# Performance work log

Measured on AMD Instinct MI355X. Metric: run time of the kernel, lower is better.

Reference implementation:

```python
import jax, jax.numpy as jnp
import numpy as np

E = 16
TOP_K = 2


def setup_inputs() -> dict:
    key = jax.random.key(0)
    k1, k2, k3, k4, k5 = jax.random.split(key, 5)
    H, I = 2048, 1408
    scale = 0.02  # typical init scale, keeps activations numerically tame
    return {
        "hidden_states": jax.random.normal(k1, (4, 2048, H), dtype=jnp.float32),
        "gate_w": jax.random.normal(k2, (H, E), dtype=jnp.float32) * scale,
        "w1": jax.random.normal(k3, (E, H, I), dtype=jnp.float32) * scale,
        "w3": jax.random.normal(k4, (E, H, I), dtype=jnp.float32) * scale,
        "w2": jax.random.normal(k5, (E, I, H), dtype=jnp.float32) * scale,
    }


def reference(hidden_states, gate_w, w1, w3, w2):
    orig_shape = hidden_states.shape
    H = orig_shape[-1]
    x = hidden_states.reshape(-1, H)          # [T, H]
    T = x.shape[0]

    # Router: gate linear -> softmax -> top-k -> renormalize (norm_expert_weight=True)
    router_logits = x @ gate_w                # [T, E]
    probs = jax.nn.softmax(router_logits, axis=-1)
    topk_w, topk_i = jax.lax.top_k(probs, TOP_K)          # [T, K]
    topk_w = topk_w / jnp.sum(topk_w, axis=-1, keepdims=True)

    # Dense combine weights [T, E] (zero for non-selected experts)
    combine = jnp.zeros((T, E), dtype=x.dtype)
    combine = combine.at[jnp.arange(T)[:, None], topk_i].add(topk_w)

    # Grouped SwiGLU experts: out = sum_e combine[:, e] * ((silu(x@w1_e) * (x@w3_e)) @ w2_e)
    out = jnp.zeros_like(x)
    for e in range(E):  # fixed small expert count
        gate_act = jax.nn.silu(x @ w1[e])     # [T, I]
        up = x @ w3[e]                        # [T, I]
        y = (gate_act * up) @ w2[e]           # [T, H]
        out = out + combine[:, e:e + 1] * y

    return out.reshape(orig_shape)
```

## Files before the change

### kernel.cpp

```cpp
#include <hip/hip_runtime.h>
#include <hip/hip_bf16.h>

#define E_ 16
#define H_ 2048
#define I_ 1408
#define BM 128
#define BN 128
#define BK 32
#define SB 48

typedef __attribute__((ext_vector_type(8))) short bf16x8;
typedef __attribute__((ext_vector_type(4))) float f32x4;

__device__ __forceinline__ int swz(int row, int e) {
  return row * SB + ((((e >> 3) + (row >> 2)) & 3) << 3) + (e & 7);
}

__device__ __forceinline__ unsigned int pk2(float a, float b) {
  __hip_bfloat162 h = __float22bfloat162_rn(make_float2(a, b));
  unsigned int u;
  __builtin_memcpy(&u, &h, 4);
  return u;
}

__device__ __forceinline__ unsigned short bf16b(float a) {
  unsigned int u = __builtin_bit_cast(unsigned int, a);
  u = (u + 0x7fffu + ((u >> 16) & 1u)) >> 16;
  return (unsigned short)u;
}

__global__ __launch_bounds__(64) void moe_router(
    const float* __restrict__ x, const float* __restrict__ gw,
    int* __restrict__ counts, int* __restrict__ list2s,
    float* __restrict__ listw, int T)
{
  const int lane = threadIdx.x;
  const int t0 = blockIdx.x * 4;
  double acc[4][16];
#pragma unroll
  for (int i = 0; i < 4; ++i)
#pragma unroll
    for (int j = 0; j < 16; ++j) acc[i][j] = 0.0;

  const float4* gw4 = (const float4*)gw;
  for (int it = 0; it < H_ / 64; ++it) {
    const int h = it * 64 + lane;
    float gv[16];
    *(float4*)&gv[0]  = gw4[h * 4 + 0];
    *(float4*)&gv[4]  = gw4[h * 4 + 1];
    *(float4*)&gv[8]  = gw4[h * 4 + 2];
    *(float4*)&gv[12] = gw4[h * 4 + 3];
    float xr[4];
#pragma unroll
    for (int i = 0; i < 4; ++i) xr[i] = x[(size_t)(t0 + i) * H_ + h];
#pragma unroll
    for (int i = 0; i < 4; ++i) {
      const double xv = (double)xr[i];
#pragma unroll
      for (int j = 0; j < 16; ++j) acc[i][j] += xv * (double)gv[j];
    }
  }
#pragma unroll
  for (int i = 0; i < 4; ++i)
#pragma unroll
    for (int j = 0; j < 16; ++j) {
      double v = acc[i][j];
#pragma unroll
      for (int m = 32; m > 0; m >>= 1) v += __shfl_xor(v, m, 64);
      acc[i][j] = v;
    }
  if (lane == 0) {
#pragma unroll
    for (int i = 0; i < 4; ++i) {
      const int t = t0 + i;
      double b1 = -1e300, b2 = -1e300;
      int i1 = 0, i2 = 0;
#pragma unroll
      for (int j = 0; j < 16; ++j) {
        const double l = acc[i][j];
        if (l > b1) { b2 = b1; i2 = i1; b1 = l; i1 = j; }
        else if (l > b2) { b2 = l; i2 = j; }
      }
      const float ex = expf((float)(b2 - b1));
      const float wa = 1.f / (1.f + ex);
      const float wb = ex / (1.f + ex);
      int p = atomicAdd(&counts[i1], 1);
      list2s[i1 * T + p] = t * 2;
      listw[i1 * T + p] = wa;
      p = atomicAdd(&counts[i2], 1);
      list2s[i2 * T + p] = t * 2 + 1;
      listw[i2 * T + p] = wb;
    }
  }
}

__global__ __launch_bounds__(256) void convert_x(
    const float* __restrict__ x, unsigned short* __restrict__ xb)
{
  const size_t idx = ((size_t)blockIdx.x * 256 + threadIdx.x) * 8;
  const float4 f0 = *(const float4*)(x + idx);
  const float4 f1 = *(const float4*)(x + idx + 4);
  uint4 o;
  o.x = pk2(f0.x, f0.y); o.y = pk2(f0.z, f0.w);
  o.z = pk2(f1.x, f1.y); o.w = pk2(f1.z, f1.w);
  *(uint4*)(xb + idx) = o;
}

__global__ __launch_bounds__(256) void convert_wT(
    const float* __restrict__ src, unsigned short* __restrict__ dst,
    int R, int C)
{
  const int e = blockIdx.z;
  src += (size_t)e * R * C;
  dst += (size_t)e * C * R;
  const int r0 = blockIdx.y * 128 + (threadIdx.x >> 4) * 8;
  const int c0 = blockIdx.x * 128 + (threadIdx.x & 15) * 8;
  float av[8][8];
#pragma unroll
  for (int j = 0; j < 8; ++j) {
    const float4 t0 = *(const float4*)(src + (size_t)(r0 + j) * C + c0);
    const float4 t1 = *(const float4*)(src + (size_t)(r0 + j) * C + c0 + 4);
    av[j][0] = t0.x; av[j][1] = t0.y; av[j][2] = t0.z; av[j][3] = t0.w;
    av[j][4] = t1.x; av[j][5] = t1.y; av[j][6] = t1.z; av[j][7] = t1.w;
  }
#pragma unroll
  for (int n = 0; n < 8; ++n) {
    uint4 o;
    o.x = pk2(av[0][n], av[1][n]);
    o.y = pk2(av[2][n], av[3][n]);
    o.z = pk2(av[4][n], av[5][n]);
    o.w = pk2(av[6][n], av[7][n]);
    *(uint4*)(dst + (size_t)(c0 + n) * R + r0) = o;
  }
}

__global__ __launch_bounds__(256) void moe_gemm1_b16(
    const unsigned short* __restrict__ xb, const unsigned short* __restrict__ w1b,
    const unsigned short* __restrict__ w3b, const int* __restrict__ counts,
    const int* __restrict__ list2s, unsigned short* __restrict__ act, int T)
{
  const int e = blockIdx.z;
  const int cnt = counts[e];
  const int m0 = blockIdx.y * BM;
  if (m0 >= cnt) return;
  const int n0 = blockIdx.x * BN;
  const unsigned short* w1e = w1b + (size_t)e * H_ * I_;
  const unsigned short* w3e = w3b + (size_t)e * H_ * I_;
  const int* lst = list2s + (size_t)e * T;

  __shared__ unsigned short As[BM * SB], B1s[BN * SB], B3s[BN * SB];

  const int tid = threadIdx.x;
  const int lane = tid & 63, wave = tid >> 6;
  const int wr = (wave >> 1) * 64, wc = (wave & 1) * 64;
  const int l16 = lane & 15, quad = lane >> 4;

  const int ar = tid >> 1, ahalf = tid & 1;
  const int apos = m0 + ar;
  const int a_t2s = lst[apos < cnt ? apos : cnt - 1];
  const unsigned short* aptr = xb + (size_t)(a_t2s >> 1) * H_ + ahalf * 16;
  const unsigned short* b1p = w1e + (size_t)(n0 + ar) * H_ + ahalf * 16;
  const unsigned short* b3p = w3e + (size_t)(n0 + ar) * H_ + ahalf * 16;

  f32x4 acc1[4][4], acc3[4][4];
  const f32x4 fz = {0.f, 0.f, 0.f, 0.f};
#pragma unroll
  for (int mi = 0; mi < 4; ++mi)
#pragma unroll
    for (int ni = 0; ni < 4; ++ni) { acc1[mi][ni] = fz; acc3[mi][ni] = fz; }

  uint4 pA0, pA1, pB10, pB11, pB30, pB31;
  pA0  = *(const uint4*)(aptr);     pA1  = *(const uint4*)(aptr + 8);
  pB10 = *(const uint4*)(b1p);      pB11 = *(const uint4*)(b1p + 8);
  pB30 = *(const uint4*)(b3p);      pB31 = *(const uint4*)(b3p + 8);

  for (int k0 = 0; k0 < H_; k0 += BK) {
    __syncthreads();
    *(uint4*)&As[swz(ar, ahalf * 16)]      = pA0;
    *(uint4*)&As[swz(ar, ahalf * 16 + 8)]  = pA1;
    *(uint4*)&B1s[swz(ar, ahalf * 16)]     = pB10;
    *(uint4*)&B1s[swz(ar, ahalf * 16 + 8)] = pB11;
    *(uint4*)&B3s[swz(ar, ahalf * 16)]     = pB30;
    *(uint4*)&B3s[swz(ar, ahalf * 16 + 8)] = pB31;
    const int kn = (k0 + BK < H_) ? k0 + BK : 0;
    pA0  = *(const uint4*)(aptr + kn);     pA1  = *(const uint4*)(aptr + kn + 8);
    pB10 = *(const uint4*)(b1p + kn);      pB11 = *(const uint4*)(b1p + kn + 8);
    pB30 = *(const uint4*)(b3p + kn);      pB31 = *(const uint4*)(b3p + kn + 8);
    __syncthreads();

    bf16x8 af[4], b1f[4], b3f[4];
#pragma unroll
    for (int mi = 0; mi < 4; ++mi)
      af[mi] = *(const bf16x8*)&As[swz(wr + mi * 16 + l16, quad * 8)];
#pragma unroll
    for (int ni = 0; ni < 4; ++ni) {
      b1f[ni] = *(const bf16x8*)&B1s[swz(wc + ni * 16 + l16, quad * 8)];
      b3f[ni] = *(const bf16x8*)&B3s[swz(wc + ni * 16 + l16, quad * 8)];
    }
#pragma unroll
    for (int mi = 0; mi < 4; ++mi)
#pragma unroll
      for (int ni = 0; ni < 4; ++ni) {
        acc1[mi][ni] = __builtin_amdgcn_mfma_f32_16x16x32_bf16(af[mi], b1f[ni], acc1[mi][ni], 0, 0, 0);
        acc3[mi][ni] = __builtin_amdgcn_mfma_f32_16x16x32_bf16(af[mi], b3f[ni], acc3[mi][ni], 0, 0, 0);
      }
  }

#pragma unroll
  for (int mi = 0; mi < 4; ++mi) {
    const int rbase = m0 + wr + mi * 16 + quad * 4;
#pragma unroll
    for (int r = 0; r < 4; ++r) {
      const int pos = rbase + r;
      if (pos < cnt) {
        const int t2s = lst[pos];
        unsigned short* op = act + (size_t)t2s * I_ + n0 + wc + l16;
#pragma unroll
        for (int ni = 0; ni < 4; ++ni) {
          const float g = acc1[mi][ni][r];
          const float u = acc3[mi][ni][r];
          const float s = g / (1.f + __expf(-g));
          op[ni * 16] = bf16b(s * u);
        }
      }
    }
  }
}

__global__ __launch_bounds__(256) void moe_gemm2_b16(
    const unsigned short* __restrict__ act, const unsigned short* __restrict__ w2b,
    const int* __restrict__ counts, const int* __restrict__ list2s,
    const float* __restrict__ listw, float* __restrict__ out, int T)
{
  const int e = blockIdx.z;
  const int cnt = counts[e];
  const int m0 = blockIdx.y * BM;
  if (m0 >= cnt) return;
  const int n0 = blockIdx.x * BN;
  const unsigned short* w2e = w2b + (size_t)e * I_ * H_;
  const int* lst = list2s + (size_t)e * T;
  const float* lw = listw + (size_t)e * T;

  __shared__ unsigned short As[BM * SB], Bs[BN * SB];

  const int tid = threadIdx.x;
  const int lane = tid & 63, wave = tid >> 6;
  const int wr = (wave >> 1) * 64, wc = (wave & 1) * 64;
  const int l16 = lane & 15, quad = lane >> 4;

  const int ar = tid >> 1, ahalf = tid & 1;
  const int apos = m0 + ar;
  const int a_t2s = lst[apos < cnt ? apos : cnt - 1];
  const unsigned short* aptr = act + (size_t)a_t2s * I_ + ahalf * 16;
  const unsigned short* bp = w2e + (size_t)(n0 + ar) * I_ + ahalf * 16;

  f32x4 acc[4][4];
  const f32x4 fz = {0.f, 0.f, 0.f, 0.f};
#pragma unroll
  for (int mi = 0; mi < 4; ++mi)
#pragma unroll
    for (int ni = 0; ni < 4; ++ni) acc[mi][ni] = fz;

  uint4 pA0, pA1, pB0, pB1;
  pA0 = *(const uint4*)(aptr);  pA1 = *(const uint4*)(aptr + 8);
  pB0 = *(const uint4*)(bp);    pB1 = *(const uint4*)(bp + 8);

  for (int k0 = 0; k0 < I_; k0 += BK) {
    __syncthreads();
    *(uint4*)&As[swz(ar, ahalf * 16)]     = pA0;
    *(uint4*)&As[swz(ar, ahalf * 16 + 8)] = pA1;
    *(uint4*)&Bs[swz(ar, ahalf * 16)]     = pB0;
    *(uint4*)&Bs[swz(ar, ahalf * 16 + 8)] = pB1;
    const int kn = (k0 + BK < I_) ? k0 + BK : 0;
    pA0 = *(const uint4*)(aptr + kn);  pA1 = *(const uint4*)(aptr + kn + 8);
    pB0 = *(const uint4*)(bp + kn);    pB1 = *(const uint4*)(bp + kn + 8);
    __syncthreads();

    bf16x8 af[4], bf[4];
#pragma unroll
    for (int mi = 0; mi < 4; ++mi)
      af[mi] = *(const bf16x8*)&As[swz(wr + mi * 16 + l16, quad * 8)];
#pragma unroll
    for (int ni = 0; ni < 4; ++ni)
      bf[ni] = *(const bf16x8*)&Bs[swz(wc + ni * 16 + l16, quad * 8)];
#pragma unroll
    for (int mi = 0; mi < 4; ++mi)
#pragma unroll
      for (int ni = 0; ni < 4; ++ni)
        acc[mi][ni] = __builtin_amdgcn_mfma_f32_16x16x32_bf16(af[mi], bf[ni], acc[mi][ni], 0, 0, 0);
  }

#pragma unroll
  for (int mi = 0; mi < 4; ++mi) {
    const int rbase = m0 + wr + mi * 16 + quad * 4;
#pragma unroll
    for (int r = 0; r < 4; ++r) {
      const int pos = rbase + r;
      if (pos < cnt) {
        const int t2s = lst[pos];
        const float wt = lw[pos];
        float* op = out + (size_t)(t2s >> 1) * H_ + n0 + wc + l16;
#pragma unroll
        for (int ni = 0; ni < 4; ++ni)
          atomicAdd(op + ni * 16, wt * acc[mi][ni][r]);
      }
    }
  }
}

__device__ __forceinline__ void stage_b(const float* __restrict__ bp,
                                        unsigned short* Bs, int bn, int bk, int ldb) {
  const float4 r0 = *(const float4*)(bp);
  const float4 r1 = *(const float4*)(bp + ldb);
  const float4 r2 = *(const float4*)(bp + 2 * ldb);
  const float4 r3 = *(const float4*)(bp + 3 * ldb);
  uint2 c;
  c.x = pk2(r0.x, r1.x); c.y = pk2(r2.x, r3.x);
  *(uint2*)&Bs[swz(bn + 0, bk)] = c;
  c.x = pk2(r0.y, r1.y); c.y = pk2(r2.y, r3.y);
  *(uint2*)&Bs[swz(bn + 1, bk)] = c;
  c.x = pk2(r0.z, r1.z); c.y = pk2(r2.z, r3.z);
  *(uint2*)&Bs[swz(bn + 2, bk)] = c;
  c.x = pk2(r0.w, r1.w); c.y = pk2(r2.w, r3.w);
  *(uint2*)&Bs[swz(bn + 3, bk)] = c;
}

__global__ __launch_bounds__(256) void moe_gemm1_f32(
    const float* __restrict__ x, const float* __restrict__ w1,
    const float* __restrict__ w3, const int* __restrict__ counts,
    const int* __restrict__ list2s, unsigned short* __restrict__ act, int T)
{
  const int e = blockIdx.z;
  const int cnt = counts[e];
  const int m0 = blockIdx.y * BM;
  if (m0 >= cnt) return;
  const int n0 = blockIdx.x * BN;
  const float* w1e = w1 + (size_t)e * H_ * I_;
  const float* w3e = w3 + (size_t)e * H_ * I_;
  const int* lst = list2s + (size_t)e * T;

  __shared__ unsigned short As[BM * SB], B1s[BN * SB], B3s[BN * SB];

  const int tid = threadIdx.x;
  const int lane = tid & 63, wave = tid >> 6;
  const int wr = (wave >> 1) * 64, wc = (wave & 1) * 64;
  const int l16 = lane & 15, quad = lane >> 4;

  const int ar = tid >> 1, ahalf = tid & 1;
  const int apos = m0 + ar;
  const int a_t2s = lst[apos < cnt ? apos : cnt - 1];
  const float* aptr = x + (size_t)(a_t2s >> 1) * H_ + ahalf * 16;

  const int nq = tid & 31, kb = tid >> 5;
  const int bn = nq * 4, bk = kb * 4;

  f32x4 acc1[4][4], acc3[4][4];
  const f32x4 fz = {0.f, 0.f, 0.f, 0.f};
#pragma unroll
  for (int mi = 0; mi < 4; ++mi)
#pragma unroll
    for (int ni = 0; ni < 4; ++ni) { acc1[mi][ni] = fz; acc3[mi][ni] = fz; }

  for (int k0 = 0; k0 < H_; k0 += BK) {
    __syncthreads();
    {
      const float4 a0 = *(const float4*)(aptr + k0);
      const float4 a1 = *(const float4*)(aptr + k0 + 4);
      const float4 a2 = *(const float4*)(aptr + k0 + 8);
      const float4 a3 = *(const float4*)(aptr + k0 + 12);
      uint4 A0, A1;
      A0.x = pk2(a0.x, a0.y); A0.y = pk2(a0.z, a0.w);
      A0.z = pk2(a1.x, a1.y); A0.w = pk2(a1.z, a1.w);
      A1.x = pk2(a2.x, a2.y); A1.y = pk2(a2.z, a2.w);
      A1.z = pk2(a3.x, a3.y); A1.w = pk2(a3.z, a3.w);
      *(uint4*)&As[swz(ar, ahalf * 16)] = A0;
      *(uint4*)&As[swz(ar, ahalf * 16 + 8)] = A1;
    }
    stage_b(w1e + (size_t)(k0 + bk) * I_ + n0 + bn, B1s, bn, bk, I_);
    stage_b(w3e + (size_t)(k0 + bk) * I_ + n0 + bn, B3s, bn, bk, I_);
    __syncthreads();

    bf16x8 af[4], b1f[4], b3f[4];
#pragma unroll
    for (int mi = 0; mi < 4; ++mi)
      af[mi] = *(const bf16x8*)&As[swz(wr + mi * 16 + l16, quad * 8)];
#pragma unroll
    for (int ni = 0; ni < 4; ++ni) {
      b1f[ni] = *(const bf16x8*)&B1s[swz(wc + ni * 16 + l16, quad * 8)];
      b3f[ni] = *(const bf16x8*)&B3s[swz(wc + ni * 16 + l16, quad * 8)];
    }
#pragma unroll
    for (int mi = 0; mi < 4; ++mi)
#pragma unroll
      for (int ni = 0; ni < 4; ++ni) {
        acc1[mi][ni] = __builtin_amdgcn_mfma_f32_16x16x32_bf16(af[mi], b1f[ni], acc1[mi][ni], 0, 0, 0);
        acc3[mi][ni] = __builtin_amdgcn_mfma_f32_16x16x32_bf16(af[mi], b3f[ni], acc3[mi][ni], 0, 0, 0);
      }
  }

#pragma unroll
  for (int mi = 0; mi < 4; ++mi) {
    const int rbase = m0 + wr + mi * 16 + quad * 4;
#pragma unroll
    for (int r = 0; r < 4; ++r) {
      const int pos = rbase + r;
      if (pos < cnt) {
        const int t2s = lst[pos];
        unsigned short* op = act + (size_t)t2s * I_ + n0 + wc + l16;
#pragma unroll
        for (int ni = 0; ni < 4; ++ni) {
          const float g = acc1[mi][ni][r];
          const float u = acc3[mi][ni][r];
          const float s = g / (1.f + __expf(-g));
          op[ni * 16] = bf16b(s * u);
        }
      }
    }
  }
}

__global__ __launch_bounds__(256) void moe_gemm2_f32(
    const unsigned short* __restrict__ act, const float* __restrict__ w2,
    const int* __restrict__ counts, const int* __restrict__ list2s,
    const float* __restrict__ listw, float* __restrict__ out, int T)
{
  const int e = blockIdx.z;
  const int cnt = counts[e];
  const int m0 = blockIdx.y * BM;
  if (m0 >= cnt) return;
  const int n0 = blockIdx.x * BN;
  const float* w2e = w2 + (size_t)e * I_ * H_;
  const int* lst = list2s + (size_t)e * T;
  const float* lw = listw + (size_t)e * T;

  __shared__ unsigned short As[BM * SB], Bs[BN * SB];

  const int tid = threadIdx.x;
  const int lane = tid & 63, wave = tid >> 6;
  const int wr = (wave >> 1) * 64, wc = (wave & 1) * 64;
  const int l16 = lane & 15, quad = lane >> 4;

  const int ar = tid >> 1, ahalf = tid & 1;
  const int apos = m0 + ar;
  const int a_t2s = lst[apos < cnt ? apos : cnt - 1];
  const unsigned short* aptr = act + (size_t)a_t2s * I_ + ahalf * 16;

  const int nq = tid & 31, kb = tid >> 5;
  const int bn = nq * 4, bk = kb * 4;

  f32x4 acc[4][4];
  const f32x4 fz = {0.f, 0.f, 0.f, 0.f};
#pragma unroll
  for (int mi = 0; mi < 4; ++mi)
#pragma unroll
    for (int ni = 0; ni < 4; ++ni) acc[mi][ni] = fz;

  for (int k0 = 0; k0 < I_; k0 += BK) {
    __syncthreads();
    {
      const uint4 A0 = *(const uint4*)(aptr + k0);
      const uint4 A1 = *(const uint4*)(aptr + k0 + 8);
      *(uint4*)&As[swz(ar, ahalf * 16)] = A0;
      *(uint4*)&As[swz(ar, ahalf * 16 + 8)] = A1;
    }
    stage_b(w2e + (size_t)(k0 + bk) * H_ + n0 + bn, Bs, bn, bk, H_);
    __syncthreads();

    bf16x8 af[4], bf[4];
#pragma unroll
    for (int mi = 0; mi < 4; ++mi)
      af[mi] = *(const bf16x8*)&As[swz(wr + mi * 16 + l16, quad * 8)];
#pragma unroll
    for (int ni = 0; ni < 4; ++ni)
      bf[ni] = *(const bf16x8*)&Bs[swz(wc + ni * 16 + l16, quad * 8)];
#pragma unroll
    for (int mi = 0; mi < 4; ++mi)
#pragma unroll
      for (int ni = 0; ni < 4; ++ni)
        acc[mi][ni] = __builtin_amdgcn_mfma_f32_16x16x32_bf16(af[mi], bf[ni], acc[mi][ni], 0, 0, 0);
  }

#pragma unroll
  for (int mi = 0; mi < 4; ++mi) {
    const int rbase = m0 + wr + mi * 16 + quad * 4;
#pragma unroll
    for (int r = 0; r < 4; ++r) {
      const int pos = rbase + r;
      if (pos < cnt) {
        const int t2s = lst[pos];
        const float wt = lw[pos];
        float* op = out + (size_t)(t2s >> 1) * H_ + n0 + wc + l16;
#pragma unroll
        for (int ni = 0; ni < 4; ++ni)
          atomicAdd(op + ni * 16, wt * acc[mi][ni][r]);
      }
    }
  }
}

extern "C" void kernel_launch(void* const* d_in, const int* in_sizes, int n_in,
                              void* d_out, int out_size, void* d_ws, size_t ws_size,
                              hipStream_t stream) {
  const float* x  = (const float*)d_in[0];
  const float* gw = (const float*)d_in[1];
  const float* w1 = (const float*)d_in[2];
  const float* w3 = (const float*)d_in[3];
  const float* w2 = (const float*)d_in[4];
  float* out = (float*)d_out;
  const int T = in_sizes[0] / H_;

  char* ws = (char*)d_ws;
  int* counts = (int*)ws;
  int* list2s = (int*)(ws + 256);
  float* listw = (float*)(ws + 256 + (size_t)E_ * T * 4);
  const size_t o_act = 256 + 2 * (size_t)E_ * T * 4;
  unsigned short* act = (unsigned short*)(ws + o_act);
  const size_t o_xb  = o_act + 2 * (size_t)T * I_ * 2;
  const size_t whi   = (size_t)E_ * H_ * I_ * 2;
  const size_t o_w1b = o_xb + (size_t)T * H_ * 2;
  const size_t o_w3b = o_w1b + whi;
  const size_t o_w2b = o_w3b + whi;
  const size_t need  = o_w2b + whi;

  hipMemsetAsync(counts, 0, 256, stream);
  hipMemsetAsync(out, 0, (size_t)out_size * sizeof(float), stream);
  moe_router<<<T / 4, 64, 0, stream>>>(x, gw, counts, list2s, listw, T);

  if (ws_size >= need) {
    unsigned short* xb  = (unsigned short*)(ws + o_xb);
    unsigned short* w1b = (unsigned short*)(ws + o_w1b);
    unsigned short* w3b = (unsigned short*)(ws + o_w3b);
    unsigned short* w2b = (unsigned short*)(ws + o_w2b);
    convert_x<<<(size_t)T * H_ / 2048, 256, 0, stream>>>(x, xb);
    convert_wT<<<dim3(I_ / 128, H_ / 128, E_), 256, 0, stream>>>(w1, w1b, H_, I_);
    convert_wT<<<dim3(I_ / 128, H_ / 128, E_), 256, 0, stream>>>(w3, w3b, H_, I_);
    convert_wT<<<dim3(H_ / 128, I_ / 128, E_), 256, 0, stream>>>(w2, w2b, I_, H_);
    moe_gemm1_b16<<<dim3(I_ / BN, T / BM, E_), 256, 0, stream>>>(xb, w1b, w3b, counts, list2s, act, T);
    moe_gemm2_b16<<<dim3(H_ / BN, T / BM, E_), 256, 0, stream>>>(act, w2b, counts, list2s, listw, out, T);
  } else {
    moe_gemm1_f32<<<dim3(I_ / BN, T / BM, E_), 256, 0, stream>>>(x, w1, w3, counts, list2s, act, T);
    moe_gemm2_f32<<<dim3(H_ / BN, T / BM, E_), 256, 0, stream>>>(act, w2, counts, list2s, listw, out, T);
  }
}
```

Baseline: 1.452 ms.

## Use direct global-to-LDS double-buffered loads and replace atomics with combine kernel

Both bf16 expert GEMMs now stage tiles with global_load_lds straight into double-buffered, XOR-swizzled shared memory, so the next tile's load overlaps the current tile's MFMA work without a register round-trip. The second GEMM writes per-slot weighted outputs to a scratch buffer (reusing the w1b region, which is no longer needed at that point) instead of issuing float atomics. A new combine kernel then sums the two top-k slots per token, and the output memset moves to the fallback path only. This adds an extra pass over a T*2*H float buffer and relies on the hardware-specific LDS load layout being correct.

```diff
diff --git a/kernel.cpp b/kernel.cpp
--- a/kernel.cpp
+++ b/kernel.cpp
@@ -27,6 +27,13 @@
   unsigned int u = __builtin_bit_cast(unsigned int, a);
   u = (u + 0x7fffu + ((u >> 16) & 1u)) >> 16;
   return (unsigned short)u;
+}
+
+__device__ __forceinline__ void gl_lds16(const unsigned short* g, unsigned short* l) {
+  __builtin_amdgcn_global_load_lds(
+      (const __attribute__((address_space(1))) unsigned int*)(const void*)(g),
+      (__attribute__((address_space(3))) unsigned int*)(void*)(l),
+      16, 0, 0);
 }
 
 __global__ __launch_bounds__(64) void moe_router(
@@ -148,19 +155,35 @@
   const unsigned short* w3e = w3b + (size_t)e * H_ * I_;
   const int* lst = list2s + (size_t)e * T;
 
-  __shared__ unsigned short As[BM * SB], B1s[BN * SB], B3s[BN * SB];
+  __shared__ __align__(16) unsigned short As[2][BM * 32];
+  __shared__ __align__(16) unsigned short B1s[2][BN * 32];
+  __shared__ __align__(16) unsigned short B3s[2][BN * 32];
 
   const int tid = threadIdx.x;
   const int lane = tid & 63, wave = tid >> 6;
   const int wr = (wave >> 1) * 64, wc = (wave & 1) * 64;
   const int l16 = lane & 15, quad = lane >> 4;
 
-  const int ar = tid >> 1, ahalf = tid & 1;
-  const int apos = m0 + ar;
-  const int a_t2s = lst[apos < cnt ? apos : cnt - 1];
-  const unsigned short* aptr = xb + (size_t)(a_t2s >> 1) * H_ + ahalf * 16;
-  const unsigned short* b1p = w1e + (size_t)(n0 + ar) * H_ + ahalf * 16;
-  const unsigned short* b3p = w3e + (size_t)(n0 + ar) * H_ + ahalf * 16;
+  const int r0 = 32 * wave;
+  const int rl = r0 + (lane >> 2);
+  const int ce = ((lane & 3) ^ ((lane >> 3) & 3)) << 3;
+  int p0 = m0 + rl;       p0 = p0 < cnt ? p0 : cnt - 1;
+  int p1 = m0 + rl + 16;  p1 = p1 < cnt ? p1 : cnt - 1;
+  const unsigned short* aS0 = xb + (size_t)(lst[p0] >> 1) * H_ + ce;
+  const unsigned short* aS1 = xb + (size_t)(lst[p1] >> 1) * H_ + ce;
+  const unsigned short* b1S0 = w1e + (size_t)(n0 + rl) * H_ + ce;
+  const unsigned short* b1S1 = w1e + (size_t)(n0 + rl + 16) * H_ + ce;
+  const unsigned short* b3S0 = w3e + (size_t)(n0 + rl) * H_ + ce;
+  const unsigned short* b3S1 = w3e + (size_t)(n0 + rl + 16) * H_ + ce;
+
+#define G1_STAGE(b, k)  {                              \
+    gl_lds16(aS0  + (k), &As[b][r0 * 32]);             \
+    gl_lds16(aS1  + (k), &As[b][(r0 + 16) * 32]);      \
+    gl_lds16(b1S0 + (k), &B1s[b][r0 * 32]);            \
+    gl_lds16(b1S1 + (k), &B1s[b][(r0 + 16) * 32]);     \
+    gl_lds16(b3S0 + (k), &B3s[b][r0 * 32]);            \
+    gl_lds16(b3S1 + (k), &B3s[b][(r0 + 16) * 32]);     \
+  }
 
   f32x4 acc1[4][4], acc3[4][4];
   const f32x4 fz = {0.f, 0.f, 0.f, 0.f};
@@ -169,42 +192,40 @@
 #pragma unroll
     for (int ni = 0; ni < 4; ++ni) { acc1[mi][ni] = fz; acc3[mi][ni] = fz; }
 
-  uint4 pA0, pA1, pB10, pB11, pB30, pB31;
-  pA0  = *(const uint4*)(aptr);     pA1  = *(const uint4*)(aptr + 8);
-  pB10 = *(const uint4*)(b1p);      pB11 = *(const uint4*)(b1p + 8);
-  pB30 = *(const uint4*)(b3p);      pB31 = *(const uint4*)(b3p + 8);
-
-  for (int k0 = 0; k0 < H_; k0 += BK) {
-    __syncthreads();
-    *(uint4*)&As[swz(ar, ahalf * 16)]      = pA0;
-    *(uint4*)&As[swz(ar, ahalf * 16 + 8)]  = pA1;
-    *(uint4*)&B1s[swz(ar, ahalf * 16)]     = pB10;
-    *(uint4*)&B1s[swz(ar, ahalf * 16 + 8)] = pB11;
-    *(uint4*)&B3s[swz(ar, ahalf * 16)]     = pB30;
-    *(uint4*)&B3s[swz(ar, ahalf * 16 + 8)] = pB31;
-    const int kn = (k0 + BK < H_) ? k0 + BK : 0;
-    pA0  = *(const uint4*)(aptr + kn);     pA1  = *(const uint4*)(aptr + kn + 8);
-    pB10 = *(const uint4*)(b1p + kn);      pB11 = *(const uint4*)(b1p + kn + 8);
-    pB30 = *(const uint4*)(b3p + kn);      pB31 = *(const uint4*)(b3p + kn + 8);
-    __syncthreads();
-
-    bf16x8 af[4], b1f[4], b3f[4];
-#pragma unroll
-    for (int mi = 0; mi < 4; ++mi)
-      af[mi] = *(const bf16x8*)&As[swz(wr + mi * 16 + l16, quad * 8)];
-#pragma unroll
-    for (int ni = 0; ni < 4; ++ni) {
-      b1f[ni] = *(const bf16x8*)&B1s[swz(wc + ni * 16 + l16, quad * 8)];
-      b3f[ni] = *(const bf16x8*)&B3s[swz(wc + ni * 16 + l16, quad * 8)];
-    }
-#pragma unroll
-    for (int mi = 0; mi < 4; ++mi)
-#pragma unroll
-      for (int ni = 0; ni < 4; ++ni) {
-        acc1[mi][ni] = __builtin_amdgcn_mfma_f32_16x16x32_bf16(af[mi], b1f[ni], acc1[mi][ni], 0, 0, 0);
-        acc3[mi][ni] = __builtin_amdgcn_mfma_f32_16x16x32_bf16(af[mi], b3f[ni], acc3[mi][ni], 0, 0, 0);
-      }
-  }
+  const int rsw = (l16 >> 1) & 3;
+  const int cA = (quad ^ rsw) << 3;
+
+#define G1_COMP(b)  {                                                          \
+    bf16x8 af[4], b1f[4], b3f[4];                                              \
+    _Pragma("unroll")                                                          \
+    for (int mi = 0; mi < 4; ++mi)                                             \
+      af[mi] = *(const bf16x8*)&As[b][(wr + mi * 16 + l16) * 32 + cA];         \
+    _Pragma("unroll")                                                          \
+    for (int ni = 0; ni < 4; ++ni) {                                           \
+      b1f[ni] = *(const bf16x8*)&B1s[b][(wc + ni * 16 + l16) * 32 + cA];       \
+      b3f[ni] = *(const bf16x8*)&B3s[b][(wc + ni * 16 + l16) * 32 + cA];       \
+    }                                                                          \
+    _Pragma("unroll")                                                          \
+    for (int mi = 0; mi < 4; ++mi)                                             \
+      _Pragma("unroll")                                                        \
+      for (int ni = 0; ni < 4; ++ni) {                                         \
+        acc1[mi][ni] = __builtin_amdgcn_mfma_f32_16x16x32_bf16(af[mi], b1f[ni], acc1[mi][ni], 0, 0, 0); \
+        acc3[mi][ni] = __builtin_amdgcn_mfma_f32_16x16x32_bf16(af[mi], b3f[ni], acc3[mi][ni], 0, 0, 0); \
+      }                                                                        \
+  }
+
+  const int NT = H_ / BK;
+  G1_STAGE(0, 0);
+  for (int t = 0; t < NT; t += 2) {
+    __syncthreads();
+    G1_STAGE(1, (t + 1) * BK);
+    G1_COMP(0);
+    __syncthreads();
+    if (t + 2 < NT) G1_STAGE(0, (t + 2) * BK);
+    G1_COMP(1);
+  }
+#undef G1_STAGE
+#undef G1_COMP
 
 #pragma unroll
   for (int mi = 0; mi < 4; ++mi) {
@@ -230,7 +251,7 @@
 __global__ __launch_bounds__(256) void moe_gemm2_b16(
     const unsigned short* __restrict__ act, const unsigned short* __restrict__ w2b,
     const int* __restrict__ counts, const int* __restrict__ list2s,
-    const float* __restrict__ listw, float* __restrict__ out, int T)
+    const float* __restrict__ listw, float* __restrict__ ys, int T)
 {
   const int e = blockIdx.z;
   const int cnt = counts[e];
@@ -241,18 +262,30 @@
   const int* lst = list2s + (size_t)e * T;
   const float* lw = listw + (size_t)e * T;
 
-  __shared__ unsigned short As[BM * SB], Bs[BN * SB];
+  __shared__ __align__(16) unsigned short As[2][BM * 32];
+  __shared__ __align__(16) unsigned short Bs[2][BN * 32];
 
   const int tid = threadIdx.x;
   const int lane = tid & 63, wave = tid >> 6;
   const int wr = (wave >> 1) * 64, wc = (wave & 1) * 64;
   const int l16 = lane & 15, quad = lane >> 4;
 
-  const int ar = tid >> 1, ahalf = tid & 1;
-  const int apos = m0 + ar;
-  const int a_t2s = lst[apos < cnt ? apos : cnt - 1];
-  const unsigned short* aptr = act + (size_t)a_t2s * I_ + ahalf * 16;
-  const unsigned short* bp = w2e + (size_t)(n0 + ar) * I_ + ahalf * 16;
+  const int r0 = 32 * wave;
+  const int rl = r0 + (lane >> 2);
+  const int ce = ((lane & 3) ^ ((lane >> 3) & 3)) << 3;
+  int p0 = m0 + rl;       p0 = p0 < cnt ? p0 : cnt - 1;
+  int p1 = m0 + rl + 16;  p1 = p1 < cnt ? p1 : cnt - 1;
+  const unsigned short* aS0 = act + (size_t)lst[p0] * I_ + ce;
+  const unsigned short* aS1 = act + (size_t)lst[p1] * I_ + ce;
+  const unsigned short* bS0 = w2e + (size_t)(n0 + rl) * I_ + ce;
+  const unsigned short* bS1 = w2e + (size_t)(n0 + rl + 16) * I_ + ce;
+
+#define G2_STAGE(b, k)  {                            \
+    gl_lds16(aS0 + (k), &As[b][r0 * 32]);            \
+    gl_lds16(aS1 + (k), &As[b][(r0 + 16) * 32]);     \
+    gl_lds16(bS0 + (k), &Bs[b][r0 * 32]);            \
+    gl_lds16(bS1 + (k), &Bs[b][(r0 + 16) * 32]);     \
+  }
 
   f32x4 acc[4][4];
   const f32x4 fz = {0.f, 0.f, 0.f, 0.f};
@@ -261,34 +294,36 @@
 #pragma unroll
     for (int ni = 0; ni < 4; ++ni) acc[mi][ni] = fz;
 
-  uint4 pA0, pA1, pB0, pB1;
-  pA0 = *(const uint4*)(aptr);  pA1 = *(const uint4*)(aptr + 8);
-  pB0 = *(const uint4*)(bp);    pB1 = *(const uint4*)(bp + 8);
-
-  for (int k0 = 0; k0 < I_; k0 += BK) {
-    __syncthreads();
-    *(uint4*)&As[swz(ar, ahalf * 16)]     = pA0;
-    *(uint4*)&As[swz(ar, ahalf * 16 + 8)] = pA1;
-    *(uint4*)&Bs[swz(ar, ahalf * 16)]     = pB0;
-    *(uint4*)&Bs[swz(ar, ahalf * 16 + 8)] = pB1;
-    const int kn = (k0 + BK < I_) ? k0 + BK : 0;
-    pA0 = *(const uint4*)(aptr + kn);  pA1 = *(const uint4*)(aptr + kn + 8);
-    pB0 = *(const uint4*)(bp + kn);    pB1 = *(const uint4*)(bp + kn + 8);
-    __syncthreads();
-
-    bf16x8 af[4], bf[4];
-#pragma unroll
-    for (int mi = 0; mi < 4; ++mi)
-      af[mi] = *(const bf16x8*)&As[swz(wr + mi * 16 + l16, quad * 8)];
-#pragma unroll
-    for (int ni = 0; ni < 4; ++ni)
-      bf[ni] = *(const bf16x8*)&Bs[swz(wc + ni * 16 + l16, quad * 8)];
-#pragma unroll
-    for (int mi = 0; mi < 4; ++mi)
-#pragma unroll
-      for (int ni = 0; ni < 4; ++ni)
-        acc[mi][ni] = __builtin_amdgcn_mfma_f32_16x16x32_bf16(af[mi], bf[ni], acc[mi][ni], 0, 0, 0);
-  }
+  const int rsw = (l16 >> 1) & 3;
+  const int cA = (quad ^ rsw) << 3;
+
+#define G2_COMP(b)  {                                                          \
+    bf16x8 af[4], bf[4];                                                       \
+    _Pragma("unroll")                                                          \
+    for (int mi = 0; mi < 4; ++mi)                                             \
+      af[mi] = *(const bf16x8*)&As[b][(wr + mi * 16 + l16) * 32 + cA];         \
+    _Pragma("unroll")                                                          \
+    for (int ni = 0; ni < 4; ++ni)                                             \
+      bf[ni] = *(const bf16x8*)&Bs[b][(wc + ni * 16 + l16) * 32 + cA];         \
+    _Pragma("unroll")                                                          \
+    for (int mi = 0; mi < 4; ++mi)                                             \
+      _Pragma("unroll")                                                        \
+      for (int ni = 0; ni < 4; ++ni)                                           \
+        acc[mi][ni] = __builtin_amdgcn_mfma_f32_16x16x32_bf16(af[mi], bf[ni], acc[mi][ni], 0, 0, 0); \
+  }
+
+  const int NT = I_ / BK;
+  G2_STAGE(0, 0);
+  for (int t = 0; t < NT; t += 2) {
+    __syncthreads();
+    G2_STAGE(1, (t + 1) * BK);
+    G2_COMP(0);
+    __syncthreads();
+    if (t + 2 < NT) G2_STAGE(0, (t + 2) * BK);
+    G2_COMP(1);
+  }
+#undef G2_STAGE
+#undef G2_COMP
 
 #pragma unroll
   for (int mi = 0; mi < 4; ++mi) {
@@ -299,29 +334,41 @@
       if (pos < cnt) {
         const int t2s = lst[pos];
         const float wt = lw[pos];
-        float* op = out + (size_t)(t2s >> 1) * H_ + n0 + wc + l16;
+        float* op = ys + (size_t)t2s * H_ + n0 + wc + l16;
 #pragma unroll
         for (int ni = 0; ni < 4; ++ni)
-          atomicAdd(op + ni * 16, wt * acc[mi][ni][r]);
+          op[ni * 16] = wt * acc[mi][ni][r];
       }
     }
   }
+}
+
+__global__ __launch_bounds__(256) void moe_combine(
+    const float* __restrict__ ys, float* __restrict__ out)
+{
+  const size_t idx = (size_t)blockIdx.x * 256 + threadIdx.x;
+  const size_t t = idx >> 9, rem = idx & 511;
+  const float4 a = ((const float4*)ys)[(t * 2) * 512 + rem];
+  const float4 b = ((const float4*)ys)[(t * 2 + 1) * 512 + rem];
+  float4 o;
+  o.x = a.x + b.x; o.y = a.y + b.y; o.z = a.z + b.z; o.w = a.w + b.w;
+  ((float4*)out)[idx] = o;
 }
 
 __device__ __forceinline__ void stage_b(const float* __restrict__ bp,
                                         unsigned short* Bs, int bn, int bk, int ldb) {
-  const float4 r0 = *(const float4*)(bp);
-  const float4 r1 = *(const float4*)(bp + ldb);
-  const float4 r2 = *(const float4*)(bp + 2 * ldb);
-  const float4 r3 = *(const float4*)(bp + 3 * ldb);
+  const float4 rr0 = *(const float4*)(bp);
+  const float4 rr1 = *(const float4*)(bp + ldb);
+  const float4 rr2 = *(const float4*)(bp + 2 * ldb);
+  const float4 rr3 = *(const float4*)(bp + 3 * ldb);
   uint2 c;
-  c.x = pk2(r0.x, r1.x); c.y = pk2(r2.x, r3.x);
+  c.x = pk2(rr0.x, rr1.x); c.y = pk2(rr2.x, rr3.x);
   *(uint2*)&Bs[swz(bn + 0, bk)] = c;
-  c.x = pk2(r0.y, r1.y); c.y = pk2(r2.y, r3.y);
+  c.x = pk2(rr0.y, rr1.y); c.y = pk2(rr2.y, rr3.y);
   *(uint2*)&Bs[swz(bn + 1, bk)] = c;
-  c.x = pk2(r0.z, r1.z); c.y = pk2(r2.z, r3.z);
+  c.x = pk2(rr0.z, rr1.z); c.y = pk2(rr2.z, rr3.z);
   *(uint2*)&Bs[swz(bn + 2, bk)] = c;
-  c.x = pk2(r0.w, r1.w); c.y = pk2(r2.w, r3.w);
+  c.x = pk2(rr0.w, rr1.w); c.y = pk2(rr2.w, rr3.w);
   *(uint2*)&Bs[swz(bn + 3, bk)] = c;
 }
 
@@ -523,7 +570,6 @@
   const size_t need  = o_w2b + whi;
 
   hipMemsetAsync(counts, 0, 256, stream);
-  hipMemsetAsync(out, 0, (size_t)out_size * sizeof(float), stream);
   moe_router<<<T / 4, 64, 0, stream>>>(x, gw, counts, list2s, listw, T);
 
   if (ws_size >= need) {
@@ -531,13 +577,16 @@
     unsigned short* w1b = (unsigned short*)(ws + o_w1b);
     unsigned short* w3b = (unsigned short*)(ws + o_w3b);
     unsigned short* w2b = (unsigned short*)(ws + o_w2b);
+    float* ys = (float*)(ws + o_w1b);
     convert_x<<<(size_t)T * H_ / 2048, 256, 0, stream>>>(x, xb);
     convert_wT<<<dim3(I_ / 128, H_ / 128, E_), 256, 0, stream>>>(w1, w1b, H_, I_);
     convert_wT<<<dim3(I_ / 128, H_ / 128, E_), 256, 0, stream>>>(w3, w3b, H_, I_);
     convert_wT<<<dim3(H_ / 128, I_ / 128, E_), 256, 0, stream>>>(w2, w2b, I_, H_);
     moe_gemm1_b16<<<dim3(I_ / BN, T / BM, E_), 256, 0, stream>>>(xb, w1b, w3b, counts, list2s, act, T);
-    moe_gemm2_b16<<<dim3(H_ / BN, T / BM, E_), 256, 0, stream>>>(act, w2b, counts, list2s, listw, out, T);
+    moe_gemm2_b16<<<dim3(H_ / BN, T / BM, E_), 256, 0, stream>>>(act, w2b, counts, list2s, listw, ys, T);
+    moe_combine<<<(size_t)T * 512 / 256, 256, 0, stream>>>(ys, out);
   } else {
+    hipMemsetAsync(out, 0, (size_t)out_size * sizeof(float), stream);
     moe_gemm1_f32<<<dim3(I_ / BN, T / BM, E_), 256, 0, stream>>>(x, w1, w3, counts, list2s, act, T);
     moe_gemm2_f32<<<dim3(H_ / BN, T / BM, E_), 256, 0, stream>>>(act, w2, counts, list2s, listw, out, T);
   }
```

New measurement: 1.498 ms. 1.03x slower.
